# Performance work log

Hardware: AMD Instinct MI355X
Metric: run time of the kernel (lower is better)

The kernel has to match this reference:

```python
import jax, jax.numpy as jnp
import numpy as np

HEADS = 8
EPS = 1e-5


def setup_inputs() -> dict:
    key = jax.random.key(0)
    B, N, C = 32, 4096, 256
    headc = C // HEADS
    x = jax.random.normal(key, (B, N, C), dtype=jnp.float32)
    return {
        "x": x,
        "kln_weight": jnp.ones((HEADS, 1, headc), dtype=jnp.float32),
        "kln_bias": jnp.zeros((HEADS, 1, headc), dtype=jnp.float32),
        "vln_weight": jnp.ones((HEADS, 1, headc), dtype=jnp.float32),
        "vln_bias": jnp.zeros((HEADS, 1, headc), dtype=jnp.float32),
    }


def _ln(t, w, b, headc):
    # Faithful to the torch module: unbiased std (ddof=1), eps added to std (not var).
    m = jnp.mean(t, axis=-1, keepdims=True)
    d = t - m
    std = jnp.sqrt(jnp.sum(d * d, axis=-1, keepdims=True) / (headc - 1))
    return w * (d / (std + EPS)) + b


def reference(x, kln_weight, kln_bias, vln_weight, vln_bias):
    B, N, C = x.shape
    headc = C // HEADS
    # [B, H, N, D]
    qkv = x.reshape(B, N, HEADS, headc).transpose(0, 2, 1, 3)
    k = _ln(qkv, kln_weight, kln_bias, headc)
    v = _ln(qkv, vln_weight, vln_bias, headc)
    # k^T v : [B, H, D, D], scaled by 1/N
    kv = jnp.einsum("bhnd,bhne->bhde", k, v) / N
    # q (k^T v): [B, H, N, D]
    out = jnp.einsum("bhnd,bhde->bhne", qkv, kv)
    out = out.transpose(0, 2, 1, 3).reshape(B, N, C)
    return out + x
```

## Files before the change

kernel.cpp:

```cpp
#include <hip/hip_runtime.h>

#define H_ 8
#define D_ 32
#define B_ 32
#define N_ 4096
#define C_ 256
#define EPS_ 1e-5f

#define SLOT_ 1088

typedef __attribute__((ext_vector_type(8))) short bf16x8;
typedef __attribute__((ext_vector_type(4))) float f32x4;

__device__ __forceinline__ short f2bf(float f) {
    unsigned u = __builtin_bit_cast(unsigned, f);
    unsigned r = (u + 0x7FFFu + ((u >> 16) & 1u)) >> 16;
    return (short)r;
}

__device__ __forceinline__ int uidx(int r, int c) {
    return r * 40 + ((r >> 3) & 3) * 16 + c;
}

__global__ __launch_bounds__(256, 4)
void k1_skv(const float* __restrict__ x, float* __restrict__ Pws)
{
    __shared__ short ubuf[256 * 40 + 64];

    const int tid  = threadIdx.x;
    const int bh   = blockIdx.x >> 2;
    const int q4   = blockIdx.x & 3;
    const int b    = bh >> 3;
    const int h    = bh & 7;
    const int lane = tid & 63;
    const int wave = tid >> 6;
    const int g    = lane >> 4;
    const int cL   = lane & 15;

    f32x4 acc[2][2] = {};
    f32x4 tq[2] = {};

    bf16x8 ones;
    #pragma unroll
    for (int j = 0; j < 8; ++j) ones[j] = (short)0x3F80;

    const float* xbase = x + ((size_t)b * N_ + q4 * 1024 + tid) * C_ + h * D_;

    float4 xA[8], xB[8];
    #pragma unroll
    for (int c = 0; c < 8; ++c)
        xA[c] = reinterpret_cast<const float4*>(xbase)[c];

    auto body = [&](const float4 (&xr)[8], float4 (&nx)[8], int it, bool pf) {
        if (pf) {
            const float* p = xbase + (size_t)(it + 1) * 256 * C_;
            #pragma unroll
            for (int c = 0; c < 8; ++c)
                nx[c] = reinterpret_cast<const float4*>(p)[c];
        }

        float sum = 0.f, sq = 0.f;
        #pragma unroll
        for (int c = 0; c < 8; ++c) {
            const float4 a = xr[c];
            sum += a.x + a.y + a.z + a.w;
            sq = fmaf(a.x, a.x, fmaf(a.y, a.y, fmaf(a.z, a.z, fmaf(a.w, a.w, sq))));
        }
        const float m   = sum * (1.f / 32.f);
        const float ss  = fmaxf(sq - sum * m, 0.f);
        const float inv = 1.f / (sqrtf(ss * (1.f / 31.f)) + EPS_);

        {
            const int base = tid * 40 + ((tid >> 3) & 3) * 16;
            #pragma unroll
            for (int q = 0; q < 4; ++q) {
                const float4 a0 = xr[q * 2 + 0];
                const float4 a1 = xr[q * 2 + 1];
                bf16x8 wv;
                wv[0] = f2bf((a0.x - m) * inv); wv[1] = f2bf((a0.y - m) * inv);
                wv[2] = f2bf((a0.z - m) * inv); wv[3] = f2bf((a0.w - m) * inv);
                wv[4] = f2bf((a1.x - m) * inv); wv[5] = f2bf((a1.y - m) * inv);
                wv[6] = f2bf((a1.z - m) * inv); wv[7] = f2bf((a1.w - m) * inv);
                *reinterpret_cast<bf16x8*>(&ubuf[base + q * 8]) = wv;
            }
        }
        asm volatile("s_waitcnt lgkmcnt(0)" ::: "memory");

        #pragma unroll
        for (int ks = 0; ks < 2; ++ks) {
            const int R0 = wave * 64 + ks * 32 + 8 * g;
            bf16x8 F0, F1;
            #pragma unroll
            for (int j = 0; j < 8; ++j) {
                const int base = uidx(R0 + j, cL);
                F0[j] = ubuf[base];
                F1[j] = ubuf[base + 16];
            }
            tq[0] = __builtin_amdgcn_mfma_f32_16x16x32_bf16(ones, F0, tq[0], 0, 0, 0);
            tq[1] = __builtin_amdgcn_mfma_f32_16x16x32_bf16(ones, F1, tq[1], 0, 0, 0);
            acc[0][0] = __builtin_amdgcn_mfma_f32_16x16x32_bf16(F0, F0, acc[0][0], 0, 0, 0);
            acc[0][1] = __builtin_amdgcn_mfma_f32_16x16x32_bf16(F0, F1, acc[0][1], 0, 0, 0);
            acc[1][0] = __builtin_amdgcn_mfma_f32_16x16x32_bf16(F1, F0, acc[1][0], 0, 0, 0);
            acc[1][1] = __builtin_amdgcn_mfma_f32_16x16x32_bf16(F1, F1, acc[1][1], 0, 0, 0);
        }
    };

    body(xA, xB, 0, true);
    body(xB, xA, 1, true);
    body(xA, xB, 2, true);
    body(xB, xA, 3, false);

    __syncthreads();
    float* sred = reinterpret_cast<float*>(ubuf);
    {
        float* dst = sred + wave * 1024;
        #pragma unroll
        for (int ca = 0; ca < 2; ++ca)
            #pragma unroll
            for (int cb = 0; cb < 2; ++cb)
                #pragma unroll
                for (int r = 0; r < 4; ++r)
                    dst[(ca * 16 + g * 4 + r) * D_ + cb * 16 + cL] = acc[ca][cb][r];
    }
    if (lane < 16) {
        sred[4096 + wave * 32 + cL]      = tq[0][0];
        sred[4096 + wave * 32 + 16 + cL] = tq[1][0];
    }
    __syncthreads();

    float* slot = Pws + (size_t)blockIdx.x * SLOT_;
    {
        const float4 c0 = *reinterpret_cast<const float4*>(&sred[tid * 4]);
        const float4 c1 = *reinterpret_cast<const float4*>(&sred[1024 + tid * 4]);
        const float4 c2 = *reinterpret_cast<const float4*>(&sred[2048 + tid * 4]);
        const float4 c3 = *reinterpret_cast<const float4*>(&sred[3072 + tid * 4]);
        float4 o;
        o.x = c0.x + c1.x + c2.x + c3.x;
        o.y = c0.y + c1.y + c2.y + c3.y;
        o.z = c0.z + c1.z + c2.z + c3.z;
        o.w = c0.w + c1.w + c2.w + c3.w;
        *reinterpret_cast<float4*>(slot + tid * 4) = o;
    }
    if (tid < D_)
        slot[1024 + tid] = sred[4096 + tid] + sred[4096 + 32 + tid]
                         + sred[4096 + 64 + tid] + sred[4096 + 96 + tid];
}

__global__ __launch_bounds__(256, 4)
void k_red(const float* __restrict__ Pws,
           const float* __restrict__ kw, const float* __restrict__ kb,
           const float* __restrict__ vw, const float* __restrict__ vb,
           float* __restrict__ kvF)
{
    const int bh  = blockIdx.x;
    const int h   = bh & 7;
    const int tid = threadIdx.x;
    const int d   = tid >> 3;
    const int e0  = (tid & 7) * 4;

    const float* P0 = Pws + (size_t)(bh * 4 + 0) * SLOT_;
    const float* P1 = Pws + (size_t)(bh * 4 + 1) * SLOT_;
    const float* P2 = Pws + (size_t)(bh * 4 + 2) * SLOT_;
    const float* P3 = Pws + (size_t)(bh * 4 + 3) * SLOT_;
    const float invN = 1.f / (float)N_;

    const float4 s0 = *reinterpret_cast<const float4*>(P0 + d * D_ + e0);
    const float4 s1 = *reinterpret_cast<const float4*>(P1 + d * D_ + e0);
    const float4 s2 = *reinterpret_cast<const float4*>(P2 + d * D_ + e0);
    const float4 s3 = *reinterpret_cast<const float4*>(P3 + d * D_ + e0);
    float Sde[4] = { s0.x + s1.x + s2.x + s3.x, s0.y + s1.y + s2.y + s3.y,
                     s0.z + s1.z + s2.z + s3.z, s0.w + s1.w + s2.w + s3.w };

    const float Td  = P0[1024 + d] + P1[1024 + d] + P2[1024 + d] + P3[1024 + d];
    const float wkd = kw[h * D_ + d];
    const float bkd = kb[h * D_ + d];

    float4 o;
    float* op = &o.x;
    #pragma unroll
    for (int j = 0; j < 4; ++j) {
        const int e = e0 + j;
        const float Te  = P0[1024 + e] + P1[1024 + e] + P2[1024 + e] + P3[1024 + e];
        const float wve = vw[h * D_ + e];
        const float bve = vb[h * D_ + e];
        op[j] = invN * (wkd * (wve * Sde[j] + bve * Td) + bkd * wve * Te)
              + bkd * bve;
    }
    *reinterpret_cast<float4*>(kvF + (size_t)bh * 1024 + tid * 4) = o;
}

__global__ __launch_bounds__(256, 4)
void k2_out(const float* __restrict__ x, const float* __restrict__ kvF,
            float* __restrict__ out)
{
    __shared__ float lds[4][2][256];

    const int tid  = threadIdx.x;
    const int lane = tid & 63;
    const int w    = tid >> 6;
    const int hloc = lane >> 5;
    const int e    = lane & 31;
    const int R0   = blockIdx.x * 64;
    const int b    = R0 >> 12;
    const int n0   = R0 & (N_ - 1);
    const int h    = 2 * w + hloc;

    const float* kvp = kvF + ((size_t)(b * H_ + h)) * 1024 + e;
    float kvc[32];
    #pragma unroll
    for (int d = 0; d < D_; ++d) kvc[d] = kvp[d * D_];

    const int lrow = lane >> 4;
    const int lcol = (lane & 15) * 4;
    const float* xg = x + ((size_t)b * N_ + n0 + lrow) * C_ + w * 64 + lcol;
    float* og = out + ((size_t)b * N_ + n0) * C_ + w * 64 + hloc * 32 + e;

    float* buf0 = &lds[w][0][0];
    float* buf1 = &lds[w][1][0];
    const int wslot = lrow * 64 + lcol;

    float4 pA = *reinterpret_cast<const float4*>(xg);
    float4 pB = *reinterpret_cast<const float4*>(xg + (size_t)4 * C_);

    #pragma unroll 4
    for (int t = 0; t < 16; ++t) {
        float* buf = (t & 1) ? buf1 : buf0;
        *reinterpret_cast<float4*>(buf + wslot) = pA;
        pA = pB;
        if (t + 2 < 16)
            pB = *reinterpret_cast<const float4*>(xg + (size_t)(t + 2) * 4 * C_);
        asm volatile("s_waitcnt lgkmcnt(0)" ::: "memory");

        #pragma unroll
        for (int r = 0; r < 4; ++r) {
            const float4* row4 =
                reinterpret_cast<const float4*>(buf + r * 64 + hloc * 32);
            float dot = 0.f;
            #pragma unroll
            for (int c = 0; c < 8; ++c) {
                const float4 a = row4[c];
                dot += a.x * kvc[c * 4 + 0] + a.y * kvc[c * 4 + 1]
                     + a.z * kvc[c * 4 + 2] + a.w * kvc[c * 4 + 3];
            }
            const float resx = buf[r * 64 + hloc * 32 + e];
            og[(size_t)(t * 4 + r) * C_] = dot + resx;
        }
    }
}

extern "C" void kernel_launch(void* const* d_in, const int* in_sizes, int n_in,
                              void* d_out, int out_size, void* d_ws, size_t ws_size,
                              hipStream_t stream)
{
    const float* x  = (const float*)d_in[0];
    const float* kw = (const float*)d_in[1];
    const float* kb = (const float*)d_in[2];
    const float* vw = (const float*)d_in[3];
    const float* vb = (const float*)d_in[4];
    float* outp = (float*)d_out;

    float* Pws = (float*)d_ws;
    float* kvF = Pws + (size_t)1024 * SLOT_;

    k1_skv<<<dim3(B_ * H_ * 4), dim3(256), 0, stream>>>(x, Pws);
    k_red<<<dim3(B_ * H_), dim3(256), 0, stream>>>(Pws, kw, kb, vw, vb, kvF);
    k2_out<<<dim3(B_ * N_ / 64), dim3(256), 0, stream>>>(x, kvF, outp);
}
```

Baseline: 83.40 us.

## Compute output projection with bf16 MFMA using hi/lo split kv matrix

The output kernel drops the per-lane FP32 dot-product loop and uses bf16 16x16x32 MFMA instructions. The kv matrix is stored as a bf16 hi/lo pair in an MFMA-friendly swizzled layout so that two MFMAs recover extra precision on the kv side. The x rows are staged into a larger 64x256 LDS tile and converted to bf16 for the A operand. This aims to cut VALU work in the memory-bound final pass, at the cost of a single bf16 rounding on q, more LDS per block and lower occupancy (launch bounds 2).

```diff
diff --git a/kernel.cpp b/kernel.cpp
--- a/kernel.cpp
+++ b/kernel.cpp
@@ -16,6 +16,9 @@
     unsigned u = __builtin_bit_cast(unsigned, f);
     unsigned r = (u + 0x7FFFu + ((u >> 16) & 1u)) >> 16;
     return (short)r;
+}
+__device__ __forceinline__ float bf2f(short s) {
+    return __builtin_bit_cast(float, ((unsigned)(unsigned short)s) << 16);
 }
 
 __device__ __forceinline__ int uidx(int r, int c) {
@@ -150,7 +153,7 @@
 void k_red(const float* __restrict__ Pws,
            const float* __restrict__ kw, const float* __restrict__ kb,
            const float* __restrict__ vw, const float* __restrict__ vb,
-           float* __restrict__ kvF)
+           short* __restrict__ kvHi, short* __restrict__ kvLo)
 {
     const int bh  = blockIdx.x;
     const int h   = bh & 7;
@@ -175,75 +178,89 @@
     const float wkd = kw[h * D_ + d];
     const float bkd = kb[h * D_ + d];
 
-    float4 o;
-    float* op = &o.x;
     #pragma unroll
     for (int j = 0; j < 4; ++j) {
         const int e = e0 + j;
         const float Te  = P0[1024 + e] + P1[1024 + e] + P2[1024 + e] + P3[1024 + e];
         const float wve = vw[h * D_ + e];
         const float bve = vb[h * D_ + e];
-        op[j] = invN * (wkd * (wve * Sde[j] + bve * Td) + bkd * wve * Te)
-              + bkd * bve;
-    }
-    *reinterpret_cast<float4*>(kvF + (size_t)bh * 1024 + tid * 4) = o;
-}
-
-__global__ __launch_bounds__(256, 4)
-void k2_out(const float* __restrict__ x, const float* __restrict__ kvF,
+        const float v = invN * (wkd * (wve * Sde[j] + bve * Td) + bkd * wve * Te)
+                      + bkd * bve;
+        const short hi = f2bf(v);
+        const short lo = f2bf(v - bf2f(hi));
+        const int hf  = e >> 4;
+        const int l   = ((d >> 3) << 4) | (e & 15);
+        const int idx = bh * 1024 + hf * 512 + l * 8 + (d & 7);
+        kvHi[idx] = hi;
+        kvLo[idx] = lo;
+    }
+}
+
+__global__ __launch_bounds__(256, 2)
+void k2_out(const float* __restrict__ x,
+            const short* __restrict__ kvHi, const short* __restrict__ kvLo,
             float* __restrict__ out)
 {
-    __shared__ float lds[4][2][256];
+    __shared__ float xt[64][256];
 
     const int tid  = threadIdx.x;
     const int lane = tid & 63;
     const int w    = tid >> 6;
-    const int hloc = lane >> 5;
-    const int e    = lane & 31;
-    const int R0   = blockIdx.x * 64;
-    const int b    = R0 >> 12;
-    const int n0   = R0 & (N_ - 1);
-    const int h    = 2 * w + hloc;
-
-    const float* kvp = kvF + ((size_t)(b * H_ + h)) * 1024 + e;
-    float kvc[32];
-    #pragma unroll
-    for (int d = 0; d < D_; ++d) kvc[d] = kvp[d * D_];
-
-    const int lrow = lane >> 4;
-    const int lcol = (lane & 15) * 4;
-    const float* xg = x + ((size_t)b * N_ + n0 + lrow) * C_ + w * 64 + lcol;
-    float* og = out + ((size_t)b * N_ + n0) * C_ + w * 64 + hloc * 32 + e;
-
-    float* buf0 = &lds[w][0][0];
-    float* buf1 = &lds[w][1][0];
-    const int wslot = lrow * 64 + lcol;
-
-    float4 pA = *reinterpret_cast<const float4*>(xg);
-    float4 pB = *reinterpret_cast<const float4*>(xg + (size_t)4 * C_);
-
-    #pragma unroll 4
-    for (int t = 0; t < 16; ++t) {
-        float* buf = (t & 1) ? buf1 : buf0;
-        *reinterpret_cast<float4*>(buf + wslot) = pA;
-        pA = pB;
-        if (t + 2 < 16)
-            pB = *reinterpret_cast<const float4*>(xg + (size_t)(t + 2) * 4 * C_);
-        asm volatile("s_waitcnt lgkmcnt(0)" ::: "memory");
-
-        #pragma unroll
-        for (int r = 0; r < 4; ++r) {
-            const float4* row4 =
-                reinterpret_cast<const float4*>(buf + r * 64 + hloc * 32);
-            float dot = 0.f;
-            #pragma unroll
-            for (int c = 0; c < 8; ++c) {
-                const float4 a = row4[c];
-                dot += a.x * kvc[c * 4 + 0] + a.y * kvc[c * 4 + 1]
-                     + a.z * kvc[c * 4 + 2] + a.w * kvc[c * 4 + 3];
+    const int g    = lane >> 4;
+    const int cL   = lane & 15;
+    const int r0   = blockIdx.x * 64;
+    const int b    = blockIdx.x >> 6;
+    const int wr   = w * 16;
+
+    bf16x8 Bhi[16], Blo[16];
+    #pragma unroll
+    for (int h = 0; h < 8; ++h)
+        #pragma unroll
+        for (int hf = 0; hf < 2; ++hf) {
+            const size_t off = (size_t)(b * H_ + h) * 1024 + hf * 512 + lane * 8;
+            Bhi[h * 2 + hf] = *reinterpret_cast<const bf16x8*>(kvHi + off);
+            Blo[h * 2 + hf] = *reinterpret_cast<const bf16x8*>(kvLo + off);
+        }
+
+    const float* gx = x + (size_t)(r0 + wr) * C_ + lane * 4;
+    {
+        float4 v[8];
+        #pragma unroll
+        for (int i = 0; i < 8; ++i)
+            v[i] = *reinterpret_cast<const float4*>(gx + (size_t)i * C_);
+        #pragma unroll
+        for (int i = 0; i < 8; ++i)
+            *reinterpret_cast<float4*>(&xt[wr + i][lane * 4]) = v[i];
+        #pragma unroll
+        for (int i = 0; i < 8; ++i)
+            v[i] = *reinterpret_cast<const float4*>(gx + (size_t)(i + 8) * C_);
+        #pragma unroll
+        for (int i = 0; i < 8; ++i)
+            *reinterpret_cast<float4*>(&xt[wr + 8 + i][lane * 4]) = v[i];
+    }
+    asm volatile("s_waitcnt lgkmcnt(0)" ::: "memory");
+    __builtin_amdgcn_sched_barrier(0);
+
+    const f32x4 zero = {0.f, 0.f, 0.f, 0.f};
+
+    #pragma unroll
+    for (int h = 0; h < 8; ++h) {
+        const float4 a0 = *reinterpret_cast<const float4*>(&xt[wr + cL][h * 32 + 8 * g]);
+        const float4 a1 = *reinterpret_cast<const float4*>(&xt[wr + cL][h * 32 + 8 * g + 4]);
+        bf16x8 A;
+        A[0] = f2bf(a0.x); A[1] = f2bf(a0.y); A[2] = f2bf(a0.z); A[3] = f2bf(a0.w);
+        A[4] = f2bf(a1.x); A[5] = f2bf(a1.y); A[6] = f2bf(a1.z); A[7] = f2bf(a1.w);
+
+        #pragma unroll
+        for (int hf = 0; hf < 2; ++hf) {
+            f32x4 Dv = __builtin_amdgcn_mfma_f32_16x16x32_bf16(A, Blo[h * 2 + hf], zero, 0, 0, 0);
+            Dv = __builtin_amdgcn_mfma_f32_16x16x32_bf16(A, Bhi[h * 2 + hf], Dv, 0, 0, 0);
+            const int col = h * 32 + hf * 16 + cL;
+            #pragma unroll
+            for (int r = 0; r < 4; ++r) {
+                const int rr = wr + 4 * g + r;
+                out[(size_t)(r0 + rr) * C_ + col] = Dv[r] + xt[rr][col];
             }
-            const float resx = buf[r * 64 + hloc * 32 + e];
-            og[(size_t)(t * 4 + r) * C_] = dot + resx;
         }
     }
 }
@@ -259,10 +276,11 @@
     const float* vb = (const float*)d_in[4];
     float* outp = (float*)d_out;
 
-    float* Pws = (float*)d_ws;
-    float* kvF = Pws + (size_t)1024 * SLOT_;
+    float* Pws  = (float*)d_ws;
+    short* kvHi = (short*)(Pws + (size_t)1024 * SLOT_);
+    short* kvLo = kvHi + (size_t)256 * 1024;
 
     k1_skv<<<dim3(B_ * H_ * 4), dim3(256), 0, stream>>>(x, Pws);
-    k_red<<<dim3(B_ * H_), dim3(256), 0, stream>>>(Pws, kw, kb, vw, vb, kvF);
-    k2_out<<<dim3(B_ * N_ / 64), dim3(256), 0, stream>>>(x, kvF, outp);
-}
+    k_red<<<dim3(B_ * H_), dim3(256), 0, stream>>>(Pws, kw, kb, vw, vb, kvHi, kvLo);
+    k2_out<<<dim3(B_ * N_ / 64), dim3(256), 0, stream>>>(x, kvHi, kvLo, outp);
+}
```

New measurement: 81.24 us. 1.03x faster.
